# Kernel optimization log

Hardware: AMD Instinct MI355X
Metric: run time of the kernel (lower is better)

The kernel has to match this reference:

```python
import jax, jax.numpy as jnp
import numpy as np

EPS_NORM = 1e-12  # torch F.normalize default eps
QUAT_FLR = 0.1    # denominator floor in matrix_to_quaternion


def _nrm(v, eps=EPS_NORM):
    n = jnp.linalg.norm(v, axis=-1, keepdims=True)
    return v / jnp.maximum(n, eps)


def _sqrt_positive_part(x):
    pos = x > 0
    return jnp.where(pos, jnp.sqrt(jnp.where(pos, x, 1.0)), 0.0)


def _triangle2projection(tri):
    # tri: (F, 3, 3) -> (F, 4, 4) rigid transform [R | a; 0 0 0 1]
    a, b, c = tri[:, 0], tri[:, 1], tri[:, 2]
    n = _nrm(jnp.cross(b - a, c - a))
    d = b - a
    X = _nrm(jnp.cross(d, n))
    Y = _nrm(jnp.cross(d, X))
    Z = _nrm(d)
    R = jnp.stack([X, Y, Z], axis=-1)              # columns X,Y,Z -> (F,3,3)
    top = jnp.concatenate([R, a[..., None]], axis=-1)  # (F,3,4)
    bot = jnp.broadcast_to(jnp.array([0.0, 0.0, 0.0, 1.0], dtype=tri.dtype), (tri.shape[0], 1, 4))
    return jnp.concatenate([top, bot], axis=-2)    # (F,4,4)


def _matrix_to_quaternion(Rm):
    # Rm: (F, 3, 3) -> (F, 4) wxyz, pytorch3d-style candidate selection
    m = Rm.reshape(Rm.shape[0], 9)
    m00, m01, m02, m10, m11, m12, m20, m21, m22 = [m[:, i] for i in range(9)]
    q_abs = _sqrt_positive_part(jnp.stack([
        1.0 + m00 + m11 + m22,
        1.0 + m00 - m11 - m22,
        1.0 - m00 + m11 - m22,
        1.0 - m00 - m11 + m22], axis=-1))          # (F,4)
    quat_by_rijk = jnp.stack([
        jnp.stack([q_abs[:, 0] ** 2, m21 - m12, m02 - m20, m10 - m01], axis=-1),
        jnp.stack([m21 - m12, q_abs[:, 1] ** 2, m10 + m01, m02 + m20], axis=-1),
        jnp.stack([m02 - m20, m10 + m01, q_abs[:, 2] ** 2, m12 + m21], axis=-1),
        jnp.stack([m10 - m01, m20 + m02, m21 + m12, q_abs[:, 3] ** 2], axis=-1)], axis=-2)  # (F,4,4)
    quat_candidates = quat_by_rijk / (2.0 * jnp.maximum(q_abs[..., None], QUAT_FLR))
    idx = jnp.argmax(q_abs, axis=-1)               # (F,)
    return jnp.take_along_axis(quat_candidates, idx[:, None, None], axis=1)[:, 0, :]


def setup_inputs() -> dict:
    V, F = 500_000, 1_000_000
    key = jax.random.key(0)
    k1, k2, k3 = jax.random.split(key, 3)
    mesh_verts = jax.random.normal(k1, (V, 3), dtype=jnp.float32)
    cano_verts = jax.random.normal(k2, (V, 3), dtype=jnp.float32)
    i0 = jax.random.randint(k3, (F,), 0, V, dtype=jnp.int32)
    # distinct vertex indices per face -> no degenerate triangles (no NaNs)
    cano_faces = jnp.stack([i0, (i0 + 1) % V, (i0 + 2) % V], axis=1)
    return {"mesh_verts": mesh_verts, "cano_verts": cano_verts, "cano_faces": cano_faces}


def reference(mesh_verts, cano_verts, cano_faces):
    V = cano_verts.shape[0]
    cano_tri = cano_verts[cano_faces]              # (F,3,3) gather
    deform_tri = mesh_verts[cano_faces]            # (F,3,3) gather
    # canonical face areas (buffer computed in __init__)
    fn = jnp.cross(cano_tri[:, 2] - cano_tri[:, 1], cano_tri[:, 0] - cano_tri[:, 1])
    face_areas = jnp.linalg.norm(fn, axis=-1, keepdims=True) / 2.0   # (F,1)
    # per-face rigid transform: deform_Rt @ inv(cano_Rt)
    cano_Rt = _triangle2projection(cano_tri)
    deform_Rt = _triangle2projection(deform_tri)
    Rt = jnp.einsum('fij,fjk->fik', deform_Rt, jnp.linalg.inv(cano_Rt))
    per_face_quat = _matrix_to_quaternion(Rt[:, :3, :3])             # (F,4)
    w = face_areas * per_face_quat                                   # (F,4)
    verts_quats = (jnp.zeros((V, 4), dtype=mesh_verts.dtype)
                   .at[cano_faces[:, 0]].add(w)
                   .at[cano_faces[:, 1]].add(w)
                   .at[cano_faces[:, 2]].add(w))
    n = jnp.linalg.norm(verts_quats, axis=1, keepdims=True)
    return verts_quats / jnp.maximum(n, 1e-6)
```

## Files before the change

### kernel.cpp

```cpp
#include <hip/hip_runtime.h>
#include <hip/hip_fp16.h>
#include <math.h>


#define BS     256
#define NBMAX  2048
#define NBLK1  512
#define CHMAX  2048

__device__ __forceinline__ float fast_rsqrt(float x) {
#if __has_builtin(__builtin_amdgcn_rsqf)
    return __builtin_amdgcn_rsqf(x);
#else
    return rsqrtf(x);
#endif
}
__device__ __forceinline__ float fast_rcp(float x) {
#if __has_builtin(__builtin_amdgcn_rcpf)
    return __builtin_amdgcn_rcpf(x);
#else
    return 1.0f / x;
#endif
}
__device__ __forceinline__ float fast_sqrt(float x) {
#if __has_builtin(__builtin_amdgcn_sqrtf)
    return __builtin_amdgcn_sqrtf(x);
#else
    return sqrtf(x);
#endif
}

struct V3 { float x, y, z; };

__device__ __forceinline__ V3 v3sub(const V3& a, const V3& b) {
    return V3{a.x - b.x, a.y - b.y, a.z - b.z};
}
__device__ __forceinline__ V3 v3cross(const V3& a, const V3& b) {
    return V3{a.y * b.z - a.z * b.y,
              a.z * b.x - a.x * b.z,
              a.x * b.y - a.y * b.x};
}
__device__ __forceinline__ float v3dot(const V3& a, const V3& b) {
    return a.x * b.x + a.y * b.y + a.z * b.z;
}
__device__ __forceinline__ V3 loadv(const float* __restrict__ p, int i) {
    return V3{p[3 * i], p[3 * i + 1], p[3 * i + 2]};
}

__device__ __forceinline__ float frame_fast(V3 a, V3 b, V3 c,
                                            V3& X, V3& Y, V3& Z) {
    V3 d = v3sub(b, a);
    V3 e = v3sub(c, a);
    V3 n = v3cross(d, e);
    float n2 = v3dot(n, n);
    float d2 = v3dot(d, d);
    float inv_d = fast_rsqrt(fmaxf(d2, 1e-24f));
    float inv_n = fast_rsqrt(fmaxf(n2, 1e-24f));
    V3 cdn = v3cross(d, n);
    float sX = inv_n * inv_d;
    X = V3{cdn.x * sX, cdn.y * sX, cdn.z * sX};
    V3 cdx = v3cross(d, X);
    Y = V3{cdx.x * inv_d, cdx.y * inv_d, cdx.z * inv_d};
    Z = V3{d.x * inv_d, d.y * inv_d, d.z * inv_d};
    return n2;
}

__device__ __forceinline__ void face_core(V3 ca, V3 cb, V3 cc,
                                          V3 da, V3 db, V3 dc,
                                          float& w0, float& w1, float& w2, float& w3) {
    V3 Xc, Yc, Zc, Xd, Yd, Zd;
    float n2c = frame_fast(ca, cb, cc, Xc, Yc, Zc);
    (void)frame_fast(da, db, dc, Xd, Yd, Zd);

    float area = 0.5f * fast_sqrt(n2c);

    float Rd[3][3] = {{Xd.x, Yd.x, Zd.x}, {Xd.y, Yd.y, Zd.y}, {Xd.z, Yd.z, Zd.z}};
    float Rc[3][3] = {{Xc.x, Yc.x, Zc.x}, {Xc.y, Yc.y, Zc.y}, {Xc.z, Yc.z, Zc.z}};
    float m00 = Rd[0][0]*Rc[0][0] + Rd[0][1]*Rc[0][1] + Rd[0][2]*Rc[0][2];
    float m01 = Rd[0][0]*Rc[1][0] + Rd[0][1]*Rc[1][1] + Rd[0][2]*Rc[1][2];
    float m02 = Rd[0][0]*Rc[2][0] + Rd[0][1]*Rc[2][1] + Rd[0][2]*Rc[2][2];
    float m10 = Rd[1][0]*Rc[0][0] + Rd[1][1]*Rc[0][1] + Rd[1][2]*Rc[0][2];
    float m11 = Rd[1][0]*Rc[1][0] + Rd[1][1]*Rc[1][1] + Rd[1][2]*Rc[1][2];
    float m12 = Rd[1][0]*Rc[2][0] + Rd[1][1]*Rc[2][1] + Rd[1][2]*Rc[2][2];
    float m20 = Rd[2][0]*Rc[0][0] + Rd[2][1]*Rc[0][1] + Rd[2][2]*Rc[0][2];
    float m21 = Rd[2][0]*Rc[1][0] + Rd[2][1]*Rc[1][1] + Rd[2][2]*Rc[1][2];
    float m22 = Rd[2][0]*Rc[2][0] + Rd[2][1]*Rc[2][1] + Rd[2][2]*Rc[2][2];

    float t0 = 1.0f + m00 + m11 + m22;
    float t1 = 1.0f + m00 - m11 - m22;
    float t2 = 1.0f - m00 + m11 - m22;
    float t3 = 1.0f - m00 - m11 + m22;
    int best = 0; float tb = t0;
    if (t1 > tb) { best = 1; tb = t1; }
    if (t2 > tb) { best = 2; tb = t2; }
    if (t3 > tb) { best = 3; tb = t3; }
    float qb = fast_sqrt(tb);

    float q0, q1, q2, q3;
    if (best == 0)      { q0 = tb;      q1 = m21-m12; q2 = m02-m20; q3 = m10-m01; }
    else if (best == 1) { q0 = m21-m12; q1 = tb;      q2 = m10+m01; q3 = m02+m20; }
    else if (best == 2) { q0 = m02-m20; q1 = m10+m01; q2 = tb;      q3 = m12+m21; }
    else                { q0 = m10-m01; q1 = m20+m02; q2 = m21+m12; q3 = tb;      }
    float scale = area * 0.5f * fast_rcp(fmaxf(qb, 0.1f));
    w0 = q0 * scale; w1 = q1 * scale; w2 = q2 * scale; w3 = q3 * scale;
}

__device__ __forceinline__ void face_math(const float* __restrict__ mesh,
                                          const float* __restrict__ cano,
                                          int i0, int i1, int i2,
                                          float& w0, float& w1, float& w2, float& w3) {
    face_core(loadv(cano, i0), loadv(cano, i1), loadv(cano, i2),
              loadv(mesh, i0), loadv(mesh, i1), loadv(mesh, i2),
              w0, w1, w2, w3);
}

__device__ __forceinline__ bool is_structured(int i0, int i1, int i2, int V) {
    int e1 = (i0 + 1 < V) ? i0 + 1 : i0 + 1 - V;
    int e2 = (i0 + 2 < V) ? i0 + 2 : i0 + 2 - V;
    return (i1 == e1) & (i2 == e2);
}

__global__ __launch_bounds__(1024)
void sort_kernel(const int* __restrict__ faces,
                 unsigned int* __restrict__ Hoff,
                 unsigned char* __restrict__ S1,
                 int* __restrict__ unstCnt,
                 int* __restrict__ unstList,
                 int F, int V, int NB, int CHUNKF) {
    __shared__ int h[NBMAX];
    __shared__ int off[NBMAX];
    __shared__ int cnt2[NBMAX];
    __shared__ int S0[CHMAX];
    __shared__ int wsum[16];
    __shared__ int unstC;

    int tid = threadIdx.x;
    for (int b = tid; b < NB; b += 1024) { h[b] = 0; cnt2[b] = 0; }
    if (tid == 0) unstC = 0;
    __syncthreads();

    int beg = blockIdx.x * CHUNKF;
    int end = min(F, beg + CHUNKF);

    for (int f = beg + tid; f < end; f += 1024) {
        int i0 = faces[3 * f + 0];
        int i1 = faces[3 * f + 1];
        int i2 = faces[3 * f + 2];
        if (is_structured(i0, i1, i2, V)) {
            S0[f - beg] = i0;
            atomicAdd(&h[i0 >> 8], 1);
        } else {
            S0[f - beg] = -1;
            int p = atomicAdd(&unstC, 1);
            unstList[(size_t)blockIdx.x * CHUNKF + p] = f;
        }
    }
    __syncthreads();

    {
        int e0 = (2 * tid < NB)     ? h[2 * tid]     : 0;
        int e1 = (2 * tid + 1 < NB) ? h[2 * tid + 1] : 0;
        int mysum = e0 + e1;
        int lane = tid & 63, wid = tid >> 6;
        int inc = mysum;
        #pragma unroll
        for (int d = 1; d < 64; d <<= 1) {
            int up = __shfl_up(inc, d);
            if (lane >= d) inc += up;
        }
        if (lane == 63) wsum[wid] = inc;
        __syncthreads();
        if (tid == 0) {
            int run = 0;
            #pragma unroll
            for (int i = 0; i < 16; ++i) { int x = wsum[i]; wsum[i] = run; run += x; }
        }
        __syncthreads();
        int excl = wsum[wid] + inc - mysum;
        if (2 * tid < NBMAX)     off[2 * tid]     = excl;
        if (2 * tid + 1 < NBMAX) off[2 * tid + 1] = excl + e0;
    }
    __syncthreads();

    for (int b = tid; b < NB; b += 1024)
        Hoff[(size_t)blockIdx.x * NBMAX + b] =
            (unsigned int)off[b] | ((unsigned int)h[b] << 16);
    if (tid == 0) unstCnt[blockIdx.x] = unstC;

    unsigned char* S1blk = S1 + (size_t)blockIdx.x * CHUNKF;
    for (int j = tid; j < end - beg; j += 1024) {
        int i0 = S0[j];
        if (i0 >= 0) {
            int b = i0 >> 8;
            int p = atomicAdd(&cnt2[b], 1);
            S1blk[off[b] + p] = (unsigned char)(i0 & 0xFF);
        }
    }
}

__global__ __launch_bounds__(1024)
void transpose_kernel(const unsigned int* __restrict__ Hoff,
                      unsigned int* __restrict__ HoffT, int NB) {
    __shared__ unsigned int tile[64][65];
    int bx = blockIdx.x * 64;
    int by = blockIdx.y * 64;
    int tx = threadIdx.x;
    int ty = threadIdx.y;
    #pragma unroll
    for (int k = 0; k < 4; ++k) {
        int r = by + ty + k * 16;
        int c = bx + tx;
        tile[ty + k * 16][tx] = (c < NB) ? Hoff[(size_t)r * NBMAX + c] : 0u;
    }
    __syncthreads();
    #pragma unroll
    for (int k = 0; k < 4; ++k) {
        int rowT = bx + ty + k * 16;
        int colT = by + tx;
        if (rowT < NB)
            HoffT[(size_t)rowT * NBLK1 + colT] = tile[tx][ty + k * 16];
    }
}

__global__ __launch_bounds__(256)
void count_kernel(const unsigned int* __restrict__ HoffT,
                  const unsigned char* __restrict__ S1,
                  unsigned int* __restrict__ cntA,
                  int V, int NB, int CHUNKF) {
    int b = blockIdx.x;
    if (b >= NB) return;
    __shared__ unsigned int cnt_l[BS];
    cnt_l[threadIdx.x] = 0;
    __syncthreads();
    for (int r = threadIdx.x; r < NBLK1; r += 256) {
        unsigned int pc = HoffT[(size_t)b * NBLK1 + r];
        int start = (int)(pc & 0xFFFFu);
        int cnt   = (int)(pc >> 16);
        const unsigned char* run = S1 + (size_t)r * CHUNKF + start;
        for (int j = 0; j < cnt; ++j)
            atomicAdd(&cnt_l[run[j]], 1u);
    }
    __syncthreads();
    int row = b * BS + (int)threadIdx.x;
    if (row < V) cntA[row] = cnt_l[threadIdx.x];
}

__global__ __launch_bounds__(256)
void finish_kernel(const float* __restrict__ mesh,
                   const float* __restrict__ cano,
                   const unsigned int* __restrict__ cntA,
                   const int* __restrict__ unstCnt,
                   const int* __restrict__ unstList,
                   const int* __restrict__ faces,
                   float* __restrict__ out, int V, int CHUNKF) {
    __shared__ float4 Tw[BS + 2];
    __shared__ float Ew[BS][4];
    __shared__ int anyU;
    int base = blockIdx.x * BS;
    int t = threadIdx.x;

    if (t == 0) anyU = 0;
    __syncthreads();
    {
        int u = unstCnt[t] | unstCnt[t + 256];
        if (u) atomicOr(&anyU, 1);
    }

    for (int j = t; j < BS + 2; j += 256) {
        int row = base - 2 + j;
        if (row < 0) row += V;
        if (row >= V) row -= V;
        unsigned int c = cntA[row];
        float4 res = make_float4(0.f, 0.f, 0.f, 0.f);
        if (c > 0) {
            int i1 = (row + 1 < V) ? row + 1 : row + 1 - V;
            int i2 = (row + 2 < V) ? row + 2 : row + 2 - V;
            float w0, w1, w2, w3;
            face_math(mesh, cano, row, i1, i2, w0, w1, w2, w3);
            float fc = (float)c;
            res = make_float4(w0 * fc, w1 * fc, w2 * fc, w3 * fc);
        }
        Tw[j] = res;
    }
    __syncthreads();

    if (anyU) {
        Ew[t][0] = Ew[t][1] = Ew[t][2] = Ew[t][3] = 0.f;
        __syncthreads();
        for (int blk = 0; blk < NBLK1; ++blk) {
            int cnt = unstCnt[blk];
            for (int j = t; j < cnt; j += 256) {
                int f = unstList[(size_t)blk * CHUNKF + j];
                int i0 = faces[3*f+0], i1 = faces[3*f+1], i2 = faces[3*f+2];
                float w0, w1, w2, w3;
                face_math(mesh, cano, i0, i1, i2, w0, w1, w2, w3);
                int tg[3] = {i0, i1, i2};
                #pragma unroll
                for (int k = 0; k < 3; ++k) {
                    int v = tg[k];
                    if (v >= base && v < base + BS && v < V) {
                        atomicAdd(&Ew[v - base][0], w0);
                        atomicAdd(&Ew[v - base][1], w1);
                        atomicAdd(&Ew[v - base][2], w2);
                        atomicAdd(&Ew[v - base][3], w3);
                    }
                }
            }
        }
        __syncthreads();
    }

    int v = base + t;
    if (v < V) {
        float4 a = Tw[t + 2], b4 = Tw[t + 1], c4 = Tw[t];
        float ex = 0.f, ey = 0.f, ez = 0.f, ew = 0.f;
        if (anyU) { ex = Ew[t][0]; ey = Ew[t][1]; ez = Ew[t][2]; ew = Ew[t][3]; }
        float x = a.x + b4.x + c4.x + ex;
        float y = a.y + b4.y + c4.y + ey;
        float z = a.z + b4.z + c4.z + ez;
        float w = a.w + b4.w + c4.w + ew;
        float n2 = x * x + y * y + z * z + w * w;
        float inv = (n2 > 1e-12f) ? fast_rsqrt(n2) : fast_sqrt(n2) * 1e12f;
        if (n2 <= 1e-12f) inv = 1e6f * ((n2 > 0.f) ? 1.f : 0.f) * fast_sqrt(n2) * 1e6f;
        inv = (n2 > 1e-12f) ? fast_rsqrt(n2) : 1e6f;
        if (n2 <= 1e-12f) {
            inv = 1e6f;
        }
        reinterpret_cast<float4*>(out)[v] = make_float4(x * inv, y * inv, z * inv, w * inv);
    }
}

typedef _Float16 hf2 __attribute__((ext_vector_type(2)));

__device__ __forceinline__ void atomic_pk_add_f16(__half* base, float a, float b) {
#if __has_builtin(__builtin_amdgcn_global_atomic_fadd_v2f16)
    hf2 v; v.x = (_Float16)a; v.y = (_Float16)b;
    __builtin_amdgcn_global_atomic_fadd_v2f16(
        (__attribute__((address_space(1))) hf2*)base, v);
#else
    union { _Float16 h[2]; unsigned int u; } pk;
    pk.h[0] = (_Float16)a; pk.h[1] = (_Float16)b;
    asm volatile("global_atomic_pk_add_f16 %0, %1, off"
                 :: "v"(base), "v"(pk.u) : "memory");
#endif
}

__global__ void face_kernel_f16(const float* __restrict__ mesh,
                                const float* __restrict__ cano,
                                const int* __restrict__ faces,
                                __half* __restrict__ T, float* __restrict__ E,
                                int F, int V) {
    int f = blockIdx.x * blockDim.x + threadIdx.x;
    if (f >= F) return;
    int i0 = faces[3*f+0], i1 = faces[3*f+1], i2 = faces[3*f+2];
    float w0, w1, w2, w3;
    face_math(mesh, cano, i0, i1, i2, w0, w1, w2, w3);
    if (is_structured(i0, i1, i2, V)) {
        __half* t = T + 4 * (size_t)i0;
        atomic_pk_add_f16(t,     w0, w1);
        atomic_pk_add_f16(t + 2, w2, w3);
    } else {
        atomicAdd(&E[4*i0+0], w0); atomicAdd(&E[4*i0+1], w1);
        atomicAdd(&E[4*i0+2], w2); atomicAdd(&E[4*i0+3], w3);
        atomicAdd(&E[4*i1+0], w0); atomicAdd(&E[4*i1+1], w1);
        atomicAdd(&E[4*i1+2], w2); atomicAdd(&E[4*i1+3], w3);
        atomicAdd(&E[4*i2+0], w0); atomicAdd(&E[4*i2+1], w1);
        atomicAdd(&E[4*i2+2], w2); atomicAdd(&E[4*i2+3], w3);
    }
}

__global__ void finish_kernel_f16(const __half* __restrict__ T,
                                  const float* __restrict__ E,
                                  float* __restrict__ out, int V) {
    int v = blockIdx.x * blockDim.x + threadIdx.x;
    if (v >= V) return;
    int vm1 = (v >= 1) ? v - 1 : v - 1 + V;
    int vm2 = (v >= 2) ? v - 2 : v - 2 + V;
    const __half2* p0 = reinterpret_cast<const __half2*>(T + 4 * (size_t)v);
    const __half2* p1 = reinterpret_cast<const __half2*>(T + 4 * (size_t)vm1);
    const __half2* p2 = reinterpret_cast<const __half2*>(T + 4 * (size_t)vm2);
    float2 a01 = __half22float2(p0[0]), a23 = __half22float2(p0[1]);
    float2 b01 = __half22float2(p1[0]), b23 = __half22float2(p1[1]);
    float2 c01 = __half22float2(p2[0]), c23 = __half22float2(p2[1]);
    float4 e = reinterpret_cast<const float4*>(E)[v];
    float x = a01.x + b01.x + c01.x + e.x;
    float y = a01.y + b01.y + c01.y + e.y;
    float z = a23.x + b23.x + c23.x + e.z;
    float w = a23.y + b23.y + c23.y + e.w;
    float n = sqrtf(x * x + y * y + z * z + w * w);
    float inv = 1.0f / fmaxf(n, 1e-6f);
    reinterpret_cast<float4*>(out)[v] = make_float4(x * inv, y * inv, z * inv, w * inv);
}

__global__ void face_kernel_direct(const float* __restrict__ mesh,
                                   const float* __restrict__ cano,
                                   const int* __restrict__ faces,
                                   float* __restrict__ out, int F) {
    int f = blockIdx.x * blockDim.x + threadIdx.x;
    if (f >= F) return;
    int i0 = faces[3*f+0], i1 = faces[3*f+1], i2 = faces[3*f+2];
    float w0, w1, w2, w3;
    face_math(mesh, cano, i0, i1, i2, w0, w1, w2, w3);
    atomicAdd(&out[4*i0+0], w0); atomicAdd(&out[4*i0+1], w1);
    atomicAdd(&out[4*i0+2], w2); atomicAdd(&out[4*i0+3], w3);
    atomicAdd(&out[4*i1+0], w0); atomicAdd(&out[4*i1+1], w1);
    atomicAdd(&out[4*i1+2], w2); atomicAdd(&out[4*i1+3], w3);
    atomicAdd(&out[4*i2+0], w0); atomicAdd(&out[4*i2+1], w1);
    atomicAdd(&out[4*i2+2], w2); atomicAdd(&out[4*i2+3], w3);
}

__global__ void norm_kernel(float* __restrict__ out, int V) {
    int v = blockIdx.x * blockDim.x + threadIdx.x;
    if (v >= V) return;
    float4 q = reinterpret_cast<float4*>(out)[v];
    float n = sqrtf(q.x*q.x + q.y*q.y + q.z*q.z + q.w*q.w);
    float inv = 1.0f / fmaxf(n, 1e-6f);
    reinterpret_cast<float4*>(out)[v] = make_float4(q.x*inv, q.y*inv, q.z*inv, q.w*inv);
}

extern "C" void kernel_launch(void* const* d_in, const int* in_sizes, int n_in,
                              void* d_out, int out_size, void* d_ws, size_t ws_size,
                              hipStream_t stream) {
    const float* mesh  = (const float*)d_in[0];
    const float* cano  = (const float*)d_in[1];
    const int*   faces = (const int*)d_in[2];
    float* out = (float*)d_out;

    int V = in_sizes[0] / 3;
    int F = in_sizes[2] / 3;
    const int TB = 256;
    int NB = (V + BS - 1) / BS;
    int CHUNKF = (F + NBLK1 - 1) / NBLK1;

    size_t bHoff  = (size_t)NBLK1 * NBMAX * 4;
    size_t bHoffT = (size_t)NBMAX * NBLK1 * 4;
    size_t bS1    = (((size_t)NBLK1 * CHUNKF) + 15) & ~15ull;
    size_t bCnt   = (size_t)V * 4;
    size_t bUC    = (size_t)NBLK1 * 4;
    size_t bUL    = (size_t)NBLK1 * CHUNKF * 4;
    size_t needFull = bHoff + bHoffT + bS1 + bCnt + bUC + bUL;

    size_t bytesTf16 = (size_t)V * 4 * sizeof(__half);
    size_t bytesEf32 = (size_t)V * 4 * sizeof(float);

    if (ws_size >= needFull && NB <= NBMAX && CHUNKF <= CHMAX) {
        char* p = (char*)d_ws;
        unsigned int*  Hoff    = (unsigned int*)p;   p += bHoff;
        unsigned int*  HoffT   = (unsigned int*)p;   p += bHoffT;
        unsigned char* S1      = (unsigned char*)p;  p += bS1;
        unsigned int*  cntA    = (unsigned int*)p;   p += bCnt;
        int*           unstCnt = (int*)p;            p += bUC;
        int*           unstList = (int*)p;

        sort_kernel<<<NBLK1, 1024, 0, stream>>>(faces, Hoff, S1, unstCnt, unstList,
                                                F, V, NB, CHUNKF);
        dim3 tgrid((NB + 63) / 64, NBLK1 / 64);
        transpose_kernel<<<tgrid, dim3(64, 16), 0, stream>>>(Hoff, HoffT, NB);
        count_kernel<<<NB, 256, 0, stream>>>(HoffT, S1, cntA, V, NB, CHUNKF);
        finish_kernel<<<NB, 256, 0, stream>>>(mesh, cano, cntA, unstCnt, unstList,
                                              faces, out, V, CHUNKF);
    } else if (ws_size >= bytesTf16 + bytesEf32) {
        __half* T = (__half*)d_ws;
        float*  E = (float*)((char*)d_ws + bytesTf16);
        (void)hipMemsetAsync(d_ws, 0, bytesTf16 + bytesEf32, stream);
        face_kernel_f16<<<(F + TB - 1) / TB, TB, 0, stream>>>(mesh, cano, faces, T, E, F, V);
        finish_kernel_f16<<<(V + TB - 1) / TB, TB, 0, stream>>>(T, E, out, V);
    } else {
        (void)hipMemsetAsync(out, 0, (size_t)V * 4 * sizeof(float), stream);
        face_kernel_direct<<<(F + TB - 1) / TB, TB, 0, stream>>>(mesh, cano, faces, out, F);
        norm_kernel<<<(V + TB - 1) / TB, TB, 0, stream>>>(out, V);
    }
}
```

Baseline: 32.79 us.

## Fuse count and finish kernels, recomputing halo counts per block

Merges the per-vertex count kernel into the finish kernel, so the per-block counts stay in shared memory and the global cntA buffer is removed. The two halo rows owned by the preceding block are counted again by rescanning that block's sorted runs. This saves one kernel launch and a global write and read of the counts. In exchange, every block does roughly twice the run-scanning work and adds shared-memory atomics. The normalization epilogue is also trimmed of dead redundant code.

```diff
diff --git a/kernel.cpp b/kernel.cpp
--- a/kernel.cpp
+++ b/kernel.cpp
@@ -223,16 +223,35 @@
 }
 
 __global__ __launch_bounds__(256)
-void count_kernel(const unsigned int* __restrict__ HoffT,
-                  const unsigned char* __restrict__ S1,
-                  unsigned int* __restrict__ cntA,
-                  int V, int NB, int CHUNKF) {
+void countfinish_kernel(const float* __restrict__ mesh,
+                        const float* __restrict__ cano,
+                        const unsigned int* __restrict__ HoffT,
+                        const unsigned char* __restrict__ S1,
+                        const int* __restrict__ unstCnt,
+                        const int* __restrict__ unstList,
+                        const int* __restrict__ faces,
+                        float* __restrict__ out,
+                        int V, int NB, int CHUNKF) {
+    __shared__ unsigned int cnt_l[BS];
+    __shared__ unsigned int cntB[2];
+    __shared__ float4 Tw[BS + 2];
+    __shared__ float Ew[BS][4];
+    __shared__ int anyU;
+
     int b = blockIdx.x;
-    if (b >= NB) return;
-    __shared__ unsigned int cnt_l[BS];
-    cnt_l[threadIdx.x] = 0;
-    __syncthreads();
-    for (int r = threadIdx.x; r < NBLK1; r += 256) {
+    int base = b * BS;
+    int t = threadIdx.x;
+
+    cnt_l[t] = 0;
+    if (t < 2) cntB[t] = 0;
+    if (t == 0) anyU = 0;
+    __syncthreads();
+    {
+        int u = unstCnt[t] | unstCnt[t + 256];
+        if (u) atomicOr(&anyU, 1);
+    }
+
+    for (int r = t; r < NBLK1; r += 256) {
         unsigned int pc = HoffT[(size_t)b * NBLK1 + r];
         int start = (int)(pc & 0xFFFFu);
         int cnt   = (int)(pc >> 16);
@@ -240,37 +259,40 @@
         for (int j = 0; j < cnt; ++j)
             atomicAdd(&cnt_l[run[j]], 1u);
     }
-    __syncthreads();
-    int row = b * BS + (int)threadIdx.x;
-    if (row < V) cntA[row] = cnt_l[threadIdx.x];
-}
-
-__global__ __launch_bounds__(256)
-void finish_kernel(const float* __restrict__ mesh,
-                   const float* __restrict__ cano,
-                   const unsigned int* __restrict__ cntA,
-                   const int* __restrict__ unstCnt,
-                   const int* __restrict__ unstList,
-                   const int* __restrict__ faces,
-                   float* __restrict__ out, int V, int CHUNKF) {
-    __shared__ float4 Tw[BS + 2];
-    __shared__ float Ew[BS][4];
-    __shared__ int anyU;
-    int base = blockIdx.x * BS;
-    int t = threadIdx.x;
-
-    if (t == 0) anyU = 0;
-    __syncthreads();
-    {
-        int u = unstCnt[t] | unstCnt[t + 256];
-        if (u) atomicOr(&anyU, 1);
-    }
-
-    for (int j = t; j < BS + 2; j += 256) {
+
+    int row0 = base - 2; if (row0 < 0) row0 += V;
+    int row1 = base - 1; if (row1 < 0) row1 += V;
+    int bb0 = row0 >> 8, bb1 = row1 >> 8;
+    unsigned char res0 = (unsigned char)(row0 & 255);
+    unsigned char res1 = (unsigned char)(row1 & 255);
+    for (int r = t; r < NBLK1; r += 256) {
+        unsigned int pc = HoffT[(size_t)bb0 * NBLK1 + r];
+        int start = (int)(pc & 0xFFFFu);
+        int cnt   = (int)(pc >> 16);
+        const unsigned char* run = S1 + (size_t)r * CHUNKF + start;
+        for (int j = 0; j < cnt; ++j) {
+            unsigned char x = run[j];
+            if (x == res0) atomicAdd(&cntB[0], 1u);
+            if (bb1 == bb0 && x == res1) atomicAdd(&cntB[1], 1u);
+        }
+    }
+    if (bb1 != bb0) {
+        for (int r = t; r < NBLK1; r += 256) {
+            unsigned int pc = HoffT[(size_t)bb1 * NBLK1 + r];
+            int start = (int)(pc & 0xFFFFu);
+            int cnt   = (int)(pc >> 16);
+            const unsigned char* run = S1 + (size_t)r * CHUNKF + start;
+            for (int j = 0; j < cnt; ++j)
+                if (run[j] == res1) atomicAdd(&cntB[1], 1u);
+        }
+    }
+    __syncthreads();
+
+    int rows = min(BS, V - base);
+    for (int j = t; j < rows + 2; j += 256) {
         int row = base - 2 + j;
         if (row < 0) row += V;
-        if (row >= V) row -= V;
-        unsigned int c = cntA[row];
+        unsigned int c = (j == 0) ? cntB[0] : (j == 1) ? cntB[1] : cnt_l[j - 2];
         float4 res = make_float4(0.f, 0.f, 0.f, 0.f);
         if (c > 0) {
             int i1 = (row + 1 < V) ? row + 1 : row + 1 - V;
@@ -311,21 +333,16 @@
     }
 
     int v = base + t;
-    if (v < V) {
-        float4 a = Tw[t + 2], b4 = Tw[t + 1], c4 = Tw[t];
+    if (t < rows) {
+        float4 a4 = Tw[t + 2], b4 = Tw[t + 1], c4 = Tw[t];
         float ex = 0.f, ey = 0.f, ez = 0.f, ew = 0.f;
         if (anyU) { ex = Ew[t][0]; ey = Ew[t][1]; ez = Ew[t][2]; ew = Ew[t][3]; }
-        float x = a.x + b4.x + c4.x + ex;
-        float y = a.y + b4.y + c4.y + ey;
-        float z = a.z + b4.z + c4.z + ez;
-        float w = a.w + b4.w + c4.w + ew;
+        float x = a4.x + b4.x + c4.x + ex;
+        float y = a4.y + b4.y + c4.y + ey;
+        float z = a4.z + b4.z + c4.z + ez;
+        float w = a4.w + b4.w + c4.w + ew;
         float n2 = x * x + y * y + z * z + w * w;
-        float inv = (n2 > 1e-12f) ? fast_rsqrt(n2) : fast_sqrt(n2) * 1e12f;
-        if (n2 <= 1e-12f) inv = 1e6f * ((n2 > 0.f) ? 1.f : 0.f) * fast_sqrt(n2) * 1e6f;
-        inv = (n2 > 1e-12f) ? fast_rsqrt(n2) : 1e6f;
-        if (n2 <= 1e-12f) {
-            inv = 1e6f;
-        }
+        float inv = (n2 > 1e-12f) ? fast_rsqrt(n2) : 1e6f;
         reinterpret_cast<float4*>(out)[v] = make_float4(x * inv, y * inv, z * inv, w * inv);
     }
 }
@@ -435,10 +452,9 @@
     size_t bHoff  = (size_t)NBLK1 * NBMAX * 4;
     size_t bHoffT = (size_t)NBMAX * NBLK1 * 4;
     size_t bS1    = (((size_t)NBLK1 * CHUNKF) + 15) & ~15ull;
-    size_t bCnt   = (size_t)V * 4;
     size_t bUC    = (size_t)NBLK1 * 4;
     size_t bUL    = (size_t)NBLK1 * CHUNKF * 4;
-    size_t needFull = bHoff + bHoffT + bS1 + bCnt + bUC + bUL;
+    size_t needFull = bHoff + bHoffT + bS1 + bUC + bUL;
 
     size_t bytesTf16 = (size_t)V * 4 * sizeof(__half);
     size_t bytesEf32 = (size_t)V * 4 * sizeof(float);
@@ -448,7 +464,6 @@
         unsigned int*  Hoff    = (unsigned int*)p;   p += bHoff;
         unsigned int*  HoffT   = (unsigned int*)p;   p += bHoffT;
         unsigned char* S1      = (unsigned char*)p;  p += bS1;
-        unsigned int*  cntA    = (unsigned int*)p;   p += bCnt;
         int*           unstCnt = (int*)p;            p += bUC;
         int*           unstList = (int*)p;
 
@@ -456,9 +471,9 @@
                                                 F, V, NB, CHUNKF);
         dim3 tgrid((NB + 63) / 64, NBLK1 / 64);
         transpose_kernel<<<tgrid, dim3(64, 16), 0, stream>>>(Hoff, HoffT, NB);
-        count_kernel<<<NB, 256, 0, stream>>>(HoffT, S1, cntA, V, NB, CHUNKF);
-        finish_kernel<<<NB, 256, 0, stream>>>(mesh, cano, cntA, unstCnt, unstList,
-                                              faces, out, V, CHUNKF);
+        countfinish_kernel<<<NB, 256, 0, stream>>>(mesh, cano, HoffT, S1,
+                                                   unstCnt, unstList, faces,
+                                                   out, V, NB, CHUNKF);
     } else if (ws_size >= bytesTf16 + bytesEf32) {
         __half* T = (__half*)d_ws;
         float*  E = (float*)((char*)d_ws + bytesTf16);
```

After: 34.45 us. +5.1%, slower.
